# Optimization experiments

Measured on AMD Instinct MI355X. Metric: run time of the kernel, lower is better.

## Reference

```python
import jax, jax.numpy as jnp
import numpy as np

A, B, M, H, E, N = 1, 32, 32, 1024, 8, 1024

def setup_inputs() -> dict:
    key = jax.random.key(0)
    k1, k2, k3 = jax.random.split(key, 3)
    hidden_4d = jax.random.normal(k1, (A, B, M, H), dtype=jnp.float32)
    sparsity = jax.random.uniform(k2, (A, B, 1, E), dtype=jnp.float32)
    weight = jax.random.normal(k3, (1, E, H, N), dtype=jnp.float32) * 0.02
    return {"hidden_4d": hidden_4d, "sparsity": sparsity, "weight": weight}

def reference(hidden_4d, sparsity, weight):
    # Original: out = einsum('abmh,ehn->abemn'); out *= mask[a,b,e,1,1]; out.sum((-2,-1))
    # The mask is constant over (m, n), so the sum fuses into the contraction:
    # contracted[a,b,e] = sum_{m,h,n} hidden[a,b,m,h] * weight[e,h,n]
    contracted = jnp.einsum('abmh,ehn->abe', hidden_4d, weight[0])  # (A,B,E)
    mask = jnp.squeeze(sparsity, axis=2)  # (A,B,E)
    return contracted * mask
```

## Files before the change

### kernel.cpp

```cpp
#include <hip/hip_runtime.h>


#define Bdim 32
#define Mdim 32
#define Hdim 1024
#define Edim 8
#define Ndim 1024

__global__ __launch_bounds__(256) void reduce_kernel(
    const float* __restrict__ hidden,
    const float* __restrict__ weight,
    float* __restrict__ ws)
{
    constexpr int NB_W = 512;
    if (blockIdx.x < NB_W) {
        const int wave = blockIdx.x * 4 + (threadIdx.x >> 6);
        const int lane = threadIdx.x & 63;
        const float4* w4 = reinterpret_cast<const float4*>(weight);
        #pragma unroll
        for (int r = 0; r < 4; ++r) {
            const int row = wave * 4 + r;
            float s = 0.f;
            #pragma unroll
            for (int j = 0; j < 4; ++j) {
                float4 v = w4[row * (Ndim / 4) + j * 64 + lane];
                s += (v.x + v.y) + (v.z + v.w);
            }
            #pragma unroll
            for (int off = 32; off > 0; off >>= 1)
                s += __shfl_xor(s, off, 64);
            if (lane == 0) ws[row] = s;
        }
    } else {
        const int idx = (blockIdx.x - NB_W) * 256 + threadIdx.x;
        const int b = idx >> 8;
        const float4* p4 = reinterpret_cast<const float4*>(hidden) + b * (Mdim * Hdim / 4) + (idx & 255);
        float4 acc = {0.f, 0.f, 0.f, 0.f};
        #pragma unroll
        for (int m = 0; m < Mdim; ++m) {
            float4 v = p4[m * (Hdim / 4)];
            acc.x += v.x; acc.y += v.y; acc.z += v.z; acc.w += v.w;
        }
        reinterpret_cast<float4*>(ws + Edim * Hdim)[idx] = acc;
    }
}

__global__ __launch_bounds__(256) void dot_kernel(
    const float* __restrict__ ws,
    const float* __restrict__ sparsity,
    float* __restrict__ out)
{
    const int o = blockIdx.x * 4 + (threadIdx.x >> 6);
    const int lane = threadIdx.x & 63;
    const int b = o >> 3;
    const int e = o & 7;
    const float4* hsum4 = reinterpret_cast<const float4*>(ws + Edim * Hdim + b * Hdim);
    const float4* wsum4 = reinterpret_cast<const float4*>(ws + e * Hdim);
    float s = 0.f;
    #pragma unroll
    for (int j = 0; j < 4; ++j) {
        const int h4 = j * 64 + lane;
        float4 a = hsum4[h4];
        float4 w = wsum4[h4];
        s += a.x * w.x + a.y * w.y + a.z * w.z + a.w * w.w;
    }
    #pragma unroll
    for (int off = 32; off > 0; off >>= 1)
        s += __shfl_xor(s, off, 64);
    if (lane == 0) out[o] = s * sparsity[o];
}

extern "C" void kernel_launch(void* const* d_in, const int* in_sizes, int n_in,
                              void* d_out, int out_size, void* d_ws, size_t ws_size,
                              hipStream_t stream) {
    const float* hidden   = (const float*)d_in[0];
    const float* sparsity = (const float*)d_in[1];
    const float* weight   = (const float*)d_in[2];
    float* out = (float*)d_out;
    float* ws  = (float*)d_ws;

    reduce_kernel<<<544, 256, 0, stream>>>(hidden, weight, ws);
    dot_kernel<<<64, 256, 0, stream>>>(ws, sparsity, out);
}
```

Baseline: 80.26 us.

## Split hidden M-reduction across all blocks and finish partial sums in dot kernel

The hidden-state sum over M was done by only 32 tail blocks, each looping over 32 rows, which likely made them the critical path. Now every one of the 512 blocks sums a pair of M rows for a slice of hidden and also reduces its weight rows, writing 16 partial sums per (b,h) to the workspace. The dot kernel then adds the 16 partials before the dot product. This balances load across blocks at the cost of extra workspace traffic (about 2 MB written and read back) and more work in the small dot kernel.

```diff
diff --git a/kernel.cpp b/kernel.cpp
--- a/kernel.cpp
+++ b/kernel.cpp
@@ -6,42 +6,45 @@
 #define Hdim 1024
 #define Edim 8
 #define Ndim 1024
+#define EH4  2048
 
 __global__ __launch_bounds__(256) void reduce_kernel(
     const float* __restrict__ hidden,
     const float* __restrict__ weight,
     float* __restrict__ ws)
 {
-    constexpr int NB_W = 512;
-    if (blockIdx.x < NB_W) {
-        const int wave = blockIdx.x * 4 + (threadIdx.x >> 6);
-        const int lane = threadIdx.x & 63;
-        const float4* w4 = reinterpret_cast<const float4*>(weight);
+    const int tid = threadIdx.x;
+
+    {
+        const int g   = blockIdx.x * 256 + tid;
+        const int p   = g >> 13;
+        const int idx = g & 8191;
+        const int b   = idx >> 8;
+        const int col = idx & 255;
+        const float4* h4 = reinterpret_cast<const float4*>(hidden);
+        const float4* v0p = h4 + b * (Mdim * Hdim / 4) + (2 * p) * (Hdim / 4) + col;
+        float4 v0 = v0p[0];
+        float4 v1 = v0p[Hdim / 4];
+        float4 s4 = {v0.x + v1.x, v0.y + v1.y, v0.z + v1.z, v0.w + v1.w};
+        reinterpret_cast<float4*>(ws)[EH4 + g] = s4;
+    }
+
+    const int wave = blockIdx.x * 4 + (tid >> 6);
+    const int lane = tid & 63;
+    const float4* w4 = reinterpret_cast<const float4*>(weight);
+    #pragma unroll
+    for (int r = 0; r < 4; ++r) {
+        const int row = wave * 4 + r;
+        float s = 0.f;
         #pragma unroll
-        for (int r = 0; r < 4; ++r) {
-            const int row = wave * 4 + r;
-            float s = 0.f;
-            #pragma unroll
-            for (int j = 0; j < 4; ++j) {
-                float4 v = w4[row * (Ndim / 4) + j * 64 + lane];
-                s += (v.x + v.y) + (v.z + v.w);
-            }
-            #pragma unroll
-            for (int off = 32; off > 0; off >>= 1)
-                s += __shfl_xor(s, off, 64);
-            if (lane == 0) ws[row] = s;
+        for (int j = 0; j < 4; ++j) {
+            float4 v = w4[row * (Ndim / 4) + j * 64 + lane];
+            s += (v.x + v.y) + (v.z + v.w);
         }
-    } else {
-        const int idx = (blockIdx.x - NB_W) * 256 + threadIdx.x;
-        const int b = idx >> 8;
-        const float4* p4 = reinterpret_cast<const float4*>(hidden) + b * (Mdim * Hdim / 4) + (idx & 255);
-        float4 acc = {0.f, 0.f, 0.f, 0.f};
         #pragma unroll
-        for (int m = 0; m < Mdim; ++m) {
-            float4 v = p4[m * (Hdim / 4)];
-            acc.x += v.x; acc.y += v.y; acc.z += v.z; acc.w += v.w;
-        }
-        reinterpret_cast<float4*>(ws + Edim * Hdim)[idx] = acc;
+        for (int off = 32; off > 0; off >>= 1)
+            s += __shfl_xor(s, off, 64);
+        if (lane == 0) ws[row] = s;
     }
 }
 
@@ -50,19 +53,24 @@
     const float* __restrict__ sparsity,
     float* __restrict__ out)
 {
-    const int o = blockIdx.x * 4 + (threadIdx.x >> 6);
+    const int o    = blockIdx.x * 4 + (threadIdx.x >> 6);
     const int lane = threadIdx.x & 63;
     const int b = o >> 3;
     const int e = o & 7;
-    const float4* hsum4 = reinterpret_cast<const float4*>(ws + Edim * Hdim + b * Hdim);
-    const float4* wsum4 = reinterpret_cast<const float4*>(ws + e * Hdim);
+    const float4* ws4 = reinterpret_cast<const float4*>(ws);
     float s = 0.f;
     #pragma unroll
     for (int j = 0; j < 4; ++j) {
-        const int h4 = j * 64 + lane;
-        float4 a = hsum4[h4];
-        float4 w = wsum4[h4];
-        s += a.x * w.x + a.y * w.y + a.z * w.z + a.w * w.w;
+        const int h4  = j * 64 + lane;
+        const int idx = b * 256 + h4;
+        float4 acc = ws4[EH4 + idx];
+        #pragma unroll
+        for (int p = 1; p < 16; ++p) {
+            float4 v = ws4[EH4 + p * 8192 + idx];
+            acc.x += v.x; acc.y += v.y; acc.z += v.z; acc.w += v.w;
+        }
+        float4 w = ws4[e * 256 + h4];
+        s += acc.x * w.x + acc.y * w.y + acc.z * w.z + acc.w * w.w;
     }
     #pragma unroll
     for (int off = 32; off > 0; off >>= 1)
@@ -79,6 +87,6 @@
     float* out = (float*)d_out;
     float* ws  = (float*)d_ws;
 
-    reduce_kernel<<<544, 256, 0, stream>>>(hidden, weight, ws);
+    reduce_kernel<<<512, 256, 0, stream>>>(hidden, weight, ws);
     dot_kernel<<<64, 256, 0, stream>>>(ws, sparsity, out);
 }
```

After: 84.63 us. +5.4%, slower.

## Fuse hidden and weight reductions with dot product into one atomic kernel

Applied to the files above, without the earlier changes.

Replaces the two-kernel pipeline (separate reductions into a workspace, then a dot kernel) with one kernel plus a memset of the output. Each block takes one expert and a 16-wide slice of H, sums hidden over M for that slice and all batches, sums the weight rows over N into shared memory, then atomically adds its partial dot product into the output. This removes the second launch and the workspace round trip. In exchange, hidden is re-read once per expert (8x redundant traffic), each read is a narrow 64-byte strided access, and it adds atomics plus a memset.

```diff
diff --git a/kernel.cpp b/kernel.cpp
--- a/kernel.cpp
+++ b/kernel.cpp
@@ -7,67 +7,70 @@
 #define Edim 8
 #define Ndim 1024
 
-__global__ __launch_bounds__(256) void reduce_kernel(
+__global__ __launch_bounds__(256) void fused_kernel(
     const float* __restrict__ hidden,
     const float* __restrict__ weight,
-    float* __restrict__ ws)
-{
-    constexpr int NB_W = 512;
-    if (blockIdx.x < NB_W) {
-        const int wave = blockIdx.x * 4 + (threadIdx.x >> 6);
-        const int lane = threadIdx.x & 63;
-        const float4* w4 = reinterpret_cast<const float4*>(weight);
-        #pragma unroll
-        for (int r = 0; r < 4; ++r) {
-            const int row = wave * 4 + r;
-            float s = 0.f;
-            #pragma unroll
-            for (int j = 0; j < 4; ++j) {
-                float4 v = w4[row * (Ndim / 4) + j * 64 + lane];
-                s += (v.x + v.y) + (v.z + v.w);
-            }
-            #pragma unroll
-            for (int off = 32; off > 0; off >>= 1)
-                s += __shfl_xor(s, off, 64);
-            if (lane == 0) ws[row] = s;
-        }
-    } else {
-        const int idx = (blockIdx.x - NB_W) * 256 + threadIdx.x;
-        const int b = idx >> 8;
-        const float4* p4 = reinterpret_cast<const float4*>(hidden) + b * (Mdim * Hdim / 4) + (idx & 255);
-        float4 acc = {0.f, 0.f, 0.f, 0.f};
-        #pragma unroll
-        for (int m = 0; m < Mdim; ++m) {
-            float4 v = p4[m * (Hdim / 4)];
-            acc.x += v.x; acc.y += v.y; acc.z += v.z; acc.w += v.w;
-        }
-        reinterpret_cast<float4*>(ws + Edim * Hdim)[idx] = acc;
-    }
-}
-
-__global__ __launch_bounds__(256) void dot_kernel(
-    const float* __restrict__ ws,
     const float* __restrict__ sparsity,
     float* __restrict__ out)
 {
-    const int o = blockIdx.x * 4 + (threadIdx.x >> 6);
-    const int lane = threadIdx.x & 63;
-    const int b = o >> 3;
-    const int e = o & 7;
-    const float4* hsum4 = reinterpret_cast<const float4*>(ws + Edim * Hdim + b * Hdim);
-    const float4* wsum4 = reinterpret_cast<const float4*>(ws + e * Hdim);
-    float s = 0.f;
+    __shared__ float4 hsA[Bdim][4];
+    __shared__ float4 hsB[Bdim][4];
+    __shared__ float  wsum_s[16];
+
+    const int tid = threadIdx.x;
+    const int e   = blockIdx.x >> 6;
+    const int h0  = (blockIdx.x & 63) * 16;
+
+    {
+        const int b    = tid >> 3;
+        const int half = (tid >> 2) & 1;
+        const int q    = tid & 3;
+        const float4* base = reinterpret_cast<const float4*>(hidden)
+                             + b * (Mdim * Hdim / 4) + (h0 >> 2) + q
+                             + half * 16 * (Hdim / 4);
+        float4 acc = {0.f, 0.f, 0.f, 0.f};
+        #pragma unroll
+        for (int k = 0; k < 16; ++k) {
+            float4 v = base[k * (Hdim / 4)];
+            acc.x += v.x; acc.y += v.y; acc.z += v.z; acc.w += v.w;
+        }
+        if (half == 0) hsA[b][q] = acc; else hsB[b][q] = acc;
+    }
+
+    const int wv   = tid >> 6;
+    const int lane = tid & 63;
+    const float4* w4 = reinterpret_cast<const float4*>(weight);
     #pragma unroll
     for (int j = 0; j < 4; ++j) {
-        const int h4 = j * 64 + lane;
-        float4 a = hsum4[h4];
-        float4 w = wsum4[h4];
-        s += a.x * w.x + a.y * w.y + a.z * w.z + a.w * w.w;
+        const int hh  = wv * 4 + j;
+        const int row = e * Hdim + h0 + hh;
+        float s = 0.f;
+        #pragma unroll
+        for (int c = 0; c < 4; ++c) {
+            float4 v = w4[row * (Ndim / 4) + c * 64 + lane];
+            s += (v.x + v.y) + (v.z + v.w);
+        }
+        #pragma unroll
+        for (int off = 32; off > 0; off >>= 1)
+            s += __shfl_xor(s, off, 64);
+        if (lane == 0) wsum_s[hh] = s;
     }
-    #pragma unroll
-    for (int off = 32; off > 0; off >>= 1)
-        s += __shfl_xor(s, off, 64);
-    if (lane == 0) out[o] = s * sparsity[o];
+    __syncthreads();
+
+    if (tid < Bdim) {
+        const int b = tid;
+        float p = 0.f;
+        #pragma unroll
+        for (int q = 0; q < 4; ++q) {
+            float4 hA = hsA[b][q];
+            float4 hB = hsB[b][q];
+            p += (hA.x + hB.x) * wsum_s[q * 4 + 0]
+               + (hA.y + hB.y) * wsum_s[q * 4 + 1]
+               + (hA.z + hB.z) * wsum_s[q * 4 + 2]
+               + (hA.w + hB.w) * wsum_s[q * 4 + 3];
+        }
+        atomicAdd(&out[b * Edim + e], p * sparsity[b * Edim + e]);
+    }
 }
 
 extern "C" void kernel_launch(void* const* d_in, const int* in_sizes, int n_in,
@@ -77,8 +80,7 @@
     const float* sparsity = (const float*)d_in[1];
     const float* weight   = (const float*)d_in[2];
     float* out = (float*)d_out;
-    float* ws  = (float*)d_ws;
 
-    reduce_kernel<<<544, 256, 0, stream>>>(hidden, weight, ws);
-    dot_kernel<<<64, 256, 0, stream>>>(ws, sparsity, out);
+    hipMemsetAsync(out, 0, out_size * sizeof(float), stream);
+    fused_kernel<<<512, 256, 0, stream>>>(hidden, weight, sparsity, out);
 }
```

After: 91.95 us. +14.6%, slower.
